# Optimization experiments

Hardware: AMD Instinct MI355X
Metric: run time of the kernel (lower is better)

## Reference

```python
import jax, jax.numpy as jnp
import numpy as np

N_NODES = 50000
N_EDGES = 800000
IN_CH = 128
HID = 128
OUT_CH = 16
N_LAYERS = 3
N_GRAPHS = 128
BN_EPS = 1e-5


def setup_inputs() -> dict:
    key = jax.random.key(0)
    ks = jax.random.split(key, 12)
    x = jax.random.normal(ks[0], (N_NODES, IN_CH), dtype=jnp.float32)
    edge_index = jax.random.randint(ks[1], (2, N_EDGES), 0, N_NODES, dtype=jnp.int64)
    batch = jnp.sort(jax.random.randint(ks[2], (N_NODES,), 0, N_GRAPHS, dtype=jnp.int64))
    s = 1.0 / np.sqrt(HID)
    W1 = jax.random.normal(ks[3], (N_LAYERS, IN_CH, HID), dtype=jnp.float32) * s
    b1 = jax.random.normal(ks[4], (N_LAYERS, HID), dtype=jnp.float32) * s
    W2 = jax.random.normal(ks[5], (N_LAYERS, HID, HID), dtype=jnp.float32) * s
    b2 = jax.random.normal(ks[6], (N_LAYERS, HID), dtype=jnp.float32) * s
    gamma = jnp.ones((N_LAYERS, HID), dtype=jnp.float32)
    beta = jnp.zeros((N_LAYERS, HID), dtype=jnp.float32)
    mean = jax.random.normal(ks[7], (N_LAYERS, HID), dtype=jnp.float32) * 0.1
    var = jax.random.uniform(ks[8], (N_LAYERS, HID), dtype=jnp.float32, minval=0.5, maxval=1.5)
    Wc = jax.random.normal(ks[9], (HID, OUT_CH), dtype=jnp.float32) * s
    bc = jax.random.normal(ks[10], (OUT_CH,), dtype=jnp.float32) * s
    return {"x": x, "edge_index": edge_index, "batch": batch, "W1": W1, "b1": b1,
            "W2": W2, "b2": b2, "gamma": gamma, "beta": beta, "mean": mean,
            "var": var, "Wc": Wc, "bc": bc}


def reference(x, edge_index, batch, W1, b1, W2, b2, gamma, beta, mean, var, Wc, bc):
    # GIN (eval mode: BN uses running stats, dropout is identity).
    src, dst = edge_index[0], edge_index[1]
    n = x.shape[0]
    h = x
    for i in range(N_LAYERS):
        # GINConv with eps=0: MLP(x + sum_{j->i} x_j)
        agg = jax.ops.segment_sum(h[src], dst, num_segments=n)  # [N, d]
        z = h + agg
        z = jnp.maximum(z @ W1[i] + b1[i], 0.0) @ W2[i] + b2[i]  # 2-layer MLP
        # BatchNorm1d (eval) + ReLU
        inv = gamma[i] * jax.lax.rsqrt(var[i] + BN_EPS)
        h = jnp.maximum((z - mean[i]) * inv + beta[i], 0.0)
    pooled = jax.ops.segment_sum(h, batch, num_segments=N_GRAPHS)  # [G, hid]
    return pooled @ Wc + bc
```

## Files before the change

kernel.cpp:

```cpp
#include <hip/hip_runtime.h>

#define N_NODES 50000
#define N_EDGES 800000
#define CH 128
#define N_GRAPHS 128
#define N_LAYERS 3
#define OUT_CH 16
#define BN_EPS 1e-5f
#define NSPLIT 32
#define NB 196
#define BCAP 4608
#define EPB 4096
#define NTILES (N_NODES / 16)
#define SSTRIDE 20
#define CB 6250
#define SB 196
#define PB 388

typedef unsigned short ushort_t;
typedef __attribute__((ext_vector_type(8))) short bf16x8;
typedef __attribute__((ext_vector_type(4))) float f32x4;

__device__ inline ushort_t f2b(float f) {
    unsigned u = __float_as_uint(f);
    unsigned r = (u + 0x7fffu + ((u >> 16) & 1u)) >> 16;
    return (ushort_t)r;
}
__device__ inline float blo(unsigned u) { return __uint_as_float(u << 16); }
__device__ inline float bhi(unsigned u) { return __uint_as_float(u & 0xffff0000u); }

__global__ __launch_bounds__(256) void setup_kernel(
    const float4* __restrict__ x, ushort4* __restrict__ xb, int* __restrict__ gcur,
    const int* __restrict__ batch, int* __restrict__ starts, float* __restrict__ outinit,
    const float* __restrict__ bc,
    const float* __restrict__ W1, const float* __restrict__ W2, ushort_t* __restrict__ Wt,
    const float* __restrict__ b1, const float* __restrict__ b2,
    const float* __restrict__ gamma, const float* __restrict__ beta,
    const float* __restrict__ mean, const float* __restrict__ var,
    float* __restrict__ scale, float* __restrict__ shift) {
    int bid = blockIdx.x, t = threadIdx.x;
    if (bid < CB) {
        int i = bid * 256 + t;
        if (i < NB) gcur[i] = 0;
        float4 v = x[i];
        ushort4 o;
        o.x = f2b(v.x); o.y = f2b(v.y); o.z = f2b(v.z); o.w = f2b(v.w);
        xb[i] = o;
    } else if (bid < CB + SB) {
        int i = (bid - CB) * 256 + t;
        if (i < N_GRAPHS * OUT_CH) outinit[i] = bc[i & (OUT_CH - 1)];
        if (i >= N_NODES) return;
        int b = batch[i];
        if (i == 0) {
            for (int g = 0; g <= b; ++g) starts[g] = 0;
        } else {
            int pb = batch[i - 1];
            for (int g = pb + 1; g <= b; ++g) starts[g] = i;
        }
        if (i == N_NODES - 1) {
            for (int g = b + 1; g <= N_GRAPHS; ++g) starts[g] = N_NODES;
        }
    } else {
        int i = (bid - CB - SB) * 256 + t;
        if (i < 6 * CH * CH) {
            int mat = i >> 14, r = i & 16383;
            int j = r & 7, bb = r >> 3;
            int lane = bb & 63, cs = bb >> 6;
            int ct = cs >> 2, ks = cs & 3;
            int n = ct * 16 + (lane & 15);
            int k = ks * 32 + (lane >> 4) * 8 + j;
            const float* Wsrc = (mat < 3) ? (W1 + (size_t)mat * CH * CH)
                                          : (W2 + (size_t)(mat - 3) * CH * CH);
            Wt[i] = f2b(Wsrc[k * CH + n]);
        } else {
            int e = i - 6 * CH * CH;
            if (e >= 6 * CH) return;
            int mat = e / CH, c = e % CH;
            if (mat < 3) {
                scale[e] = 1.f;
                shift[e] = b1[mat * CH + c];
            } else {
                int l = mat - 3;
                float inv = gamma[l * CH + c] * rsqrtf(var[l * CH + c] + BN_EPS);
                scale[e] = inv;
                shift[e] = (b2[l * CH + c] - mean[l * CH + c]) * inv + beta[l * CH + c];
            }
        }
    }
}

__global__ __launch_bounds__(256) void bin_kernel(const int* __restrict__ src,
                                                  const int* __restrict__ dst,
                                                  int* __restrict__ gcur,
                                                  unsigned* __restrict__ gbuck) {
    __shared__ int lcnt[256];
    __shared__ int lpref[256];
    __shared__ int lpos[NB];
    __shared__ int lbase[NB];
    __shared__ unsigned stage[EPB];
    __shared__ unsigned char sbk[EPB];
    int t = threadIdx.x;
    int e0 = blockIdx.x * EPB;
    int nloc = N_EDGES - e0; if (nloc > EPB) nloc = EPB;

    lcnt[t] = 0;
    __syncthreads();

    int2 ed[16];
    #pragma unroll
    for (int j = 0; j < 16; ++j) {
        int i = j * 256 + t;
        if (i < nloc) {
            ed[j].x = src[e0 + i];
            ed[j].y = dst[e0 + i];
            atomicAdd(&lcnt[ed[j].y >> 8], 1);
        } else ed[j].y = -1;
    }
    __syncthreads();
    int v = lcnt[t];
    lpref[t] = v;
    __syncthreads();
    for (int off = 1; off < 256; off <<= 1) {
        int y = (t >= off) ? lpref[t - off] : 0;
        __syncthreads();
        lpref[t] += y;
        __syncthreads();
    }
    int excl = lpref[t] - v;
    __syncthreads();
    lpref[t] = excl;
    if (t < NB) {
        lpos[t] = excl;
        lbase[t] = atomicAdd(&gcur[t], v);
    }
    __syncthreads();
    #pragma unroll
    for (int j = 0; j < 16; ++j) {
        if (ed[j].y >= 0) {
            int b = ed[j].y >> 8;
            int slot = atomicAdd(&lpos[b], 1);
            stage[slot] = (unsigned)ed[j].x | ((unsigned)(ed[j].y & 255) << 16);
            sbk[slot] = (unsigned char)b;
        }
    }
    __syncthreads();
    for (int i = t; i < nloc; i += 256) {
        int b = sbk[i];
        gbuck[(size_t)b * BCAP + lbase[b] + (i - lpref[b])] = stage[i];
    }
}

__global__ __launch_bounds__(256) void place_kernel(const int* __restrict__ gcur,
                                                    const unsigned* __restrict__ gbuck,
                                                    int* __restrict__ rowptr,
                                                    ushort_t* __restrict__ esrc) {
    __shared__ ushort_t ssrc[BCAP];
    __shared__ unsigned char sd[BCAP];
    __shared__ int outS[BCAP];
    __shared__ int cnt[256], pref[256], cur[256];
    __shared__ int sscan[256];
    int b = blockIdx.x, t = threadIdx.x;
    int gv = (t < NB) ? gcur[t] : 0;
    sscan[t] = gv;
    cnt[t] = 0;
    __syncthreads();
    for (int off = 1; off < 256; off <<= 1) {
        int y = (t >= off) ? sscan[t - off] : 0;
        __syncthreads();
        sscan[t] += y;
        __syncthreads();
    }
    int nb = gcur[b];
    int base = sscan[b] - nb;
    for (int i = t; i < nb; i += 256) {
        unsigned p = gbuck[(size_t)b * BCAP + i];
        ssrc[i] = (ushort_t)(p & 0xffffu);
        int dl = (p >> 16) & 0xff;
        sd[i] = (unsigned char)dl;
        atomicAdd(&cnt[dl], 1);
    }
    __syncthreads();
    int v = cnt[t];
    pref[t] = v;
    __syncthreads();
    for (int off = 1; off < 256; off <<= 1) {
        int y = (t >= off) ? pref[t - off] : 0;
        __syncthreads();
        pref[t] += y;
        __syncthreads();
    }
    int excl = pref[t] - v;
    __syncthreads();
    pref[t] = excl;
    cur[t] = 0;
    int idx = (b << 8) + t;
    if (idx < N_NODES) rowptr[idx] = base + excl;
    if (b == NB - 1 && t == 0) rowptr[N_NODES] = N_EDGES;
    __syncthreads();
    for (int i = t; i < nb; i += 256) {
        int dl = sd[i];
        int p = pref[dl] + atomicAdd(&cur[dl], 1);
        outS[p] = ssrc[i];
    }
    __syncthreads();
    for (int i = t; i < nb; i += 256)
        esrc[base + i] = (ushort_t)outS[i];
}

__global__ __launch_bounds__(512, 8) void layer_kernel(
    const unsigned* __restrict__ h2, const int* __restrict__ rowptr,
    const ushort_t* __restrict__ esrc,
    const ushort_t* __restrict__ Wf1, const ushort_t* __restrict__ Wf2,
    const float* __restrict__ shift1, const float* __restrict__ scale2,
    const float* __restrict__ shift2, ushort_t* __restrict__ hout) {
    __shared__ unsigned zt[16][68];
    __shared__ ushort_t sS[CH * SSTRIDE];

    int t = threadIdx.x;
    int wave = t >> 6, lane = t & 63;
    int quad = lane >> 4, l16 = lane & 15;
    int row0 = blockIdx.x * 16;

    for (int nn = 0; nn < 2; ++nn) {
        int node = row0 + wave * 2 + nn;
        unsigned self = h2[(size_t)node * 64 + lane];
        float ax = blo(self), ay = bhi(self);
        int e = rowptr[node], end = rowptr[node + 1];
        for (; e + 16 <= end; e += 16) {
            unsigned u[16];
            #pragma unroll
            for (int j = 0; j < 16; ++j) {
                int s = esrc[e + j];
                u[j] = h2[(size_t)s * 64 + lane];
            }
            #pragma unroll
            for (int j = 0; j < 16; ++j) { ax += blo(u[j]); ay += bhi(u[j]); }
        }
        for (; e + 8 <= end; e += 8) {
            unsigned u[8];
            #pragma unroll
            for (int j = 0; j < 8; ++j) {
                int s = esrc[e + j];
                u[j] = h2[(size_t)s * 64 + lane];
            }
            #pragma unroll
            for (int j = 0; j < 8; ++j) { ax += blo(u[j]); ay += bhi(u[j]); }
        }
        for (; e + 4 <= end; e += 4) {
            unsigned u[4];
            #pragma unroll
            for (int j = 0; j < 4; ++j) {
                int s = esrc[e + j];
                u[j] = h2[(size_t)s * 64 + lane];
            }
            #pragma unroll
            for (int j = 0; j < 4; ++j) { ax += blo(u[j]); ay += bhi(u[j]); }
        }
        for (; e < end; ++e) {
            unsigned u = h2[(size_t)esrc[e] * 64 + lane];
            ax += blo(u); ay += bhi(u);
        }
        zt[wave * 2 + nn][lane] = ((unsigned)f2b(ay) << 16) | (unsigned)f2b(ax);
    }
    __syncthreads();

    {
        bf16x8 af[4];
        #pragma unroll
        for (int ks = 0; ks < 4; ++ks)
            af[ks] = *(const bf16x8*)((const ushort_t*)&zt[l16][0] + ks * 32 + quad * 8);
        bf16x8 w1[4];
        #pragma unroll
        for (int ks = 0; ks < 4; ++ks)
            w1[ks] = *(const bf16x8*)(Wf1 + ((size_t)(wave * 4 + ks) * 64 + lane) * 8);
        f32x4 acc = (f32x4){0.f, 0.f, 0.f, 0.f};
        #pragma unroll
        for (int ks = 0; ks < 4; ++ks)
            acc = __builtin_amdgcn_mfma_f32_16x16x32_bf16(af[ks], w1[ks], acc, 0, 0, 0);
        int k = wave * 16 + l16;
        float sh = shift1[k];
        uint2 p;
        p.x = ((unsigned)f2b(fmaxf(acc[1] + sh, 0.f)) << 16)
            |  (unsigned)f2b(fmaxf(acc[0] + sh, 0.f));
        p.y = ((unsigned)f2b(fmaxf(acc[3] + sh, 0.f)) << 16)
            |  (unsigned)f2b(fmaxf(acc[2] + sh, 0.f));
        *(uint2*)&sS[k * SSTRIDE + quad * 4] = p;
    }
    __syncthreads();

    {
        bf16x8 af2[4];
        #pragma unroll
        for (int ks = 0; ks < 4; ++ks)
            #pragma unroll
            for (int j = 0; j < 8; ++j)
                af2[ks][j] = (short)sS[(ks * 32 + quad * 8 + j) * SSTRIDE + l16];
        bf16x8 w2[4];
        #pragma unroll
        for (int ks = 0; ks < 4; ++ks)
            w2[ks] = *(const bf16x8*)(Wf2 + ((size_t)(wave * 4 + ks) * 64 + lane) * 8);
        f32x4 acc = (f32x4){0.f, 0.f, 0.f, 0.f};
        #pragma unroll
        for (int ks = 0; ks < 4; ++ks)
            acc = __builtin_amdgcn_mfma_f32_16x16x32_bf16(af2[ks], w2[ks], acc, 0, 0, 0);
        int col = wave * 16 + l16;
        float sc = scale2[col], sh = shift2[col];
        #pragma unroll
        for (int r = 0; r < 4; ++r) {
            int row = row0 + quad * 4 + r;
            hout[(size_t)row * CH + col] = f2b(fmaxf(acc[r] * sc + sh, 0.f));
        }
    }
}

__global__ __launch_bounds__(64) void pool_kernel(const unsigned* __restrict__ h2,
                                                  const int* __restrict__ starts,
                                                  const float* __restrict__ Wc,
                                                  float* __restrict__ out) {
    int g = blockIdx.x / NSPLIT, s = blockIdx.x % NSPLIT;
    int c = threadIdx.x;
    int beg = starts[g], end = starts[g + 1];
    float s0 = 0.f, s1 = 0.f;
    for (int n = beg + s; n < end; n += NSPLIT) {
        unsigned u = h2[(size_t)n * 64 + c];
        s0 += blo(u); s1 += bhi(u);
    }
    float p[OUT_CH];
    #pragma unroll
    for (int o = 0; o < OUT_CH; ++o)
        p[o] = s0 * Wc[(2 * c) * OUT_CH + o] + s1 * Wc[(2 * c + 1) * OUT_CH + o];
    #pragma unroll
    for (int o = 0; o < OUT_CH; ++o) {
        p[o] += __shfl_xor(p[o], 1);
        p[o] += __shfl_xor(p[o], 2);
        p[o] += __shfl_xor(p[o], 4);
        p[o] += __shfl_xor(p[o], 8);
        p[o] += __shfl_xor(p[o], 16);
        p[o] += __shfl_xor(p[o], 32);
    }
    if (c == 0) {
        #pragma unroll
        for (int o = 0; o < OUT_CH; ++o)
            atomicAdd(&out[g * OUT_CH + o], p[o]);
    }
}

extern "C" void kernel_launch(void* const* d_in, const int* in_sizes, int n_in,
                              void* d_out, int out_size, void* d_ws, size_t ws_size,
                              hipStream_t stream) {
    const float* x     = (const float*)d_in[0];
    const int*   eidx  = (const int*)d_in[1];
    const int*   batch = (const int*)d_in[2];
    const float* W1    = (const float*)d_in[3];
    const float* b1    = (const float*)d_in[4];
    const float* W2    = (const float*)d_in[5];
    const float* b2    = (const float*)d_in[6];
    const float* gamma = (const float*)d_in[7];
    const float* beta  = (const float*)d_in[8];
    const float* mean  = (const float*)d_in[9];
    const float* var   = (const float*)d_in[10];
    const float* Wc    = (const float*)d_in[11];
    const float* bc    = (const float*)d_in[12];
    float* out = (float*)d_out;

    const int* src = eidx;
    const int* dst = eidx + N_EDGES;

    char* w = (char*)d_ws;
    size_t off = 0;
    auto alloc = [&](size_t bytes) { void* p = w + off; off += (bytes + 255) & ~(size_t)255; return p; };
    int*      gcur   = (int*)alloc(NB * 4);
    unsigned* gbuck  = (unsigned*)alloc((size_t)NB * BCAP * 4);
    int*      rowptr = (int*)alloc((N_NODES + 1) * 4);
    ushort_t* esrc   = (ushort_t*)alloc(N_EDGES * 2);
    int*      starts = (int*)alloc((N_GRAPHS + 1) * 4);
    ushort_t* Bh     = (ushort_t*)alloc((size_t)N_NODES * CH * 2);
    ushort_t* Bz     = (ushort_t*)alloc((size_t)N_NODES * CH * 2);
    ushort_t* Wt     = (ushort_t*)alloc((size_t)6 * CH * CH * 2);
    float*    scale  = (float*)alloc(6 * CH * 4);
    float*    shift  = (float*)alloc(6 * CH * 4);
    (void)ws_size; (void)n_in; (void)in_sizes; (void)out_size;

    setup_kernel<<<CB + SB + PB, 256, 0, stream>>>(
        (const float4*)x, (ushort4*)Bh, gcur,
        batch, starts, out, bc,
        W1, W2, Wt, b1, b2, gamma, beta, mean, var, scale, shift);
    bin_kernel<<<(N_EDGES + EPB - 1) / EPB, 256, 0, stream>>>(src, dst, gcur, gbuck);
    place_kernel<<<NB, 256, 0, stream>>>(gcur, gbuck, rowptr, esrc);

    ushort_t* bufA = Bh;
    ushort_t* bufB = Bz;
    for (int i = 0; i < N_LAYERS; ++i) {
        layer_kernel<<<NTILES, 512, 0, stream>>>((const unsigned*)bufA, rowptr, esrc,
                                                 Wt + (size_t)i * CH * CH,
                                                 Wt + (size_t)(3 + i) * CH * CH,
                                                 shift + i * CH,
                                                 scale + (3 + i) * CH,
                                                 shift + (3 + i) * CH,
                                                 bufB);
        ushort_t* tmp = bufA; bufA = bufB; bufB = tmp;
    }

    pool_kernel<<<N_GRAPHS * NSPLIT, 64, 0, stream>>>((const unsigned*)bufA, starts, Wc, out);
}
```

Before: 269.4 us.

## Fuse graph pooling into last GIN layer and interleave two-node gather

The last layer kernel now accumulates its post-BN activations straight into a per-graph pooled buffer with atomics, skipping the bf16 write of the final hidden state. A small classifier kernel then applies Wc and bc, which replaces the starts-based pool kernel and the starts setup. The neighbour gather now processes both of a wave's nodes in one interleaved loop with predicated 16-wide batches, so more loads are in flight. The pooling path adds float atomics and depends on batch being sorted for its fast path, and the predicated loads may raise register pressure.

```diff
diff --git a/kernel.cpp b/kernel.cpp
--- a/kernel.cpp
+++ b/kernel.cpp
@@ -7,7 +7,6 @@
 #define N_LAYERS 3
 #define OUT_CH 16
 #define BN_EPS 1e-5f
-#define NSPLIT 32
 #define NB 196
 #define BCAP 4608
 #define EPB 4096
@@ -31,8 +30,7 @@
 
 __global__ __launch_bounds__(256) void setup_kernel(
     const float4* __restrict__ x, ushort4* __restrict__ xb, int* __restrict__ gcur,
-    const int* __restrict__ batch, int* __restrict__ starts, float* __restrict__ outinit,
-    const float* __restrict__ bc,
+    float* __restrict__ pooled,
     const float* __restrict__ W1, const float* __restrict__ W2, ushort_t* __restrict__ Wt,
     const float* __restrict__ b1, const float* __restrict__ b2,
     const float* __restrict__ gamma, const float* __restrict__ beta,
@@ -42,26 +40,13 @@
     if (bid < CB) {
         int i = bid * 256 + t;
         if (i < NB) gcur[i] = 0;
+        if (i < N_GRAPHS * CH) pooled[i] = 0.f;
         float4 v = x[i];
         ushort4 o;
         o.x = f2b(v.x); o.y = f2b(v.y); o.z = f2b(v.z); o.w = f2b(v.w);
         xb[i] = o;
-    } else if (bid < CB + SB) {
+    } else {
         int i = (bid - CB) * 256 + t;
-        if (i < N_GRAPHS * OUT_CH) outinit[i] = bc[i & (OUT_CH - 1)];
-        if (i >= N_NODES) return;
-        int b = batch[i];
-        if (i == 0) {
-            for (int g = 0; g <= b; ++g) starts[g] = 0;
-        } else {
-            int pb = batch[i - 1];
-            for (int g = pb + 1; g <= b; ++g) starts[g] = i;
-        }
-        if (i == N_NODES - 1) {
-            for (int g = b + 1; g <= N_GRAPHS; ++g) starts[g] = N_NODES;
-        }
-    } else {
-        int i = (bid - CB - SB) * 256 + t;
         if (i < 6 * CH * CH) {
             int mat = i >> 14, r = i & 16383;
             int j = r & 7, bb = r >> 3;
@@ -212,7 +197,8 @@
     const ushort_t* __restrict__ esrc,
     const ushort_t* __restrict__ Wf1, const ushort_t* __restrict__ Wf2,
     const float* __restrict__ shift1, const float* __restrict__ scale2,
-    const float* __restrict__ shift2, ushort_t* __restrict__ hout) {
+    const float* __restrict__ shift2, ushort_t* __restrict__ hout,
+    const int* __restrict__ batch, float* __restrict__ pooled, int do_pool) {
     __shared__ unsigned zt[16][68];
     __shared__ ushort_t sS[CH * SSTRIDE];
 
@@ -221,46 +207,35 @@
     int quad = lane >> 4, l16 = lane & 15;
     int row0 = blockIdx.x * 16;
 
-    for (int nn = 0; nn < 2; ++nn) {
-        int node = row0 + wave * 2 + nn;
-        unsigned self = h2[(size_t)node * 64 + lane];
-        float ax = blo(self), ay = bhi(self);
-        int e = rowptr[node], end = rowptr[node + 1];
-        for (; e + 16 <= end; e += 16) {
-            unsigned u[16];
-            #pragma unroll
-            for (int j = 0; j < 16; ++j) {
-                int s = esrc[e + j];
-                u[j] = h2[(size_t)s * 64 + lane];
-            }
-            #pragma unroll
-            for (int j = 0; j < 16; ++j) { ax += blo(u[j]); ay += bhi(u[j]); }
+    {
+        int nodeA = row0 + wave * 2;
+        int nodeB = nodeA + 1;
+        unsigned selfA = h2[(size_t)nodeA * 64 + lane];
+        unsigned selfB = h2[(size_t)nodeB * 64 + lane];
+        float axA = blo(selfA), ayA = bhi(selfA);
+        float axB = blo(selfB), ayB = bhi(selfB);
+        int eA = rowptr[nodeA], endA = rowptr[nodeA + 1];
+        int eB = rowptr[nodeB], endB = rowptr[nodeB + 1];
+        while (eA < endA || eB < endB) {
+            int nA = endA - eA; if (nA > 16) nA = 16;
+            int nB = endB - eB; if (nB > 16) nB = 16;
+            unsigned uA[16], uB[16];
+            #pragma unroll
+            for (int j = 0; j < 16; ++j)
+                if (j < nA) uA[j] = h2[(size_t)esrc[eA + j] * 64 + lane];
+            #pragma unroll
+            for (int j = 0; j < 16; ++j)
+                if (j < nB) uB[j] = h2[(size_t)esrc[eB + j] * 64 + lane];
+            #pragma unroll
+            for (int j = 0; j < 16; ++j)
+                if (j < nA) { axA += blo(uA[j]); ayA += bhi(uA[j]); }
+            #pragma unroll
+            for (int j = 0; j < 16; ++j)
+                if (j < nB) { axB += blo(uB[j]); ayB += bhi(uB[j]); }
+            eA += nA; eB += nB;
         }
-        for (; e + 8 <= end; e += 8) {
-            unsigned u[8];
-            #pragma unroll
-            for (int j = 0; j < 8; ++j) {
-                int s = esrc[e + j];
-                u[j] = h2[(size_t)s * 64 + lane];
-            }
-            #pragma unroll
-            for (int j = 0; j < 8; ++j) { ax += blo(u[j]); ay += bhi(u[j]); }
-        }
-        for (; e + 4 <= end; e += 4) {
-            unsigned u[4];
-            #pragma unroll
-            for (int j = 0; j < 4; ++j) {
-                int s = esrc[e + j];
-                u[j] = h2[(size_t)s * 64 + lane];
-            }
-            #pragma unroll
-            for (int j = 0; j < 4; ++j) { ax += blo(u[j]); ay += bhi(u[j]); }
-        }
-        for (; e < end; ++e) {
-            unsigned u = h2[(size_t)esrc[e] * 64 + lane];
-            ax += blo(u); ay += bhi(u);
-        }
-        zt[wave * 2 + nn][lane] = ((unsigned)f2b(ay) << 16) | (unsigned)f2b(ax);
+        zt[wave * 2][lane]     = ((unsigned)f2b(ayA) << 16) | (unsigned)f2b(axA);
+        zt[wave * 2 + 1][lane] = ((unsigned)f2b(ayB) << 16) | (unsigned)f2b(axB);
     }
     __syncthreads();
 
@@ -305,44 +280,44 @@
             acc = __builtin_amdgcn_mfma_f32_16x16x32_bf16(af2[ks], w2[ks], acc, 0, 0, 0);
         int col = wave * 16 + l16;
         float sc = scale2[col], sh = shift2[col];
-        #pragma unroll
-        for (int r = 0; r < 4; ++r) {
-            int row = row0 + quad * 4 + r;
-            hout[(size_t)row * CH + col] = f2b(fmaxf(acc[r] * sc + sh, 0.f));
+        float hv[4];
+        #pragma unroll
+        for (int r = 0; r < 4; ++r)
+            hv[r] = fmaxf(acc[r] * sc + sh, 0.f);
+        if (!do_pool) {
+            #pragma unroll
+            for (int r = 0; r < 4; ++r) {
+                int row = row0 + quad * 4 + r;
+                hout[(size_t)row * CH + col] = f2b(hv[r]);
+            }
+        } else {
+            int g0 = batch[row0], g15 = batch[row0 + 15];
+            if (g0 == g15) {
+                float s = hv[0] + hv[1] + hv[2] + hv[3];
+                s += __shfl_xor(s, 16);
+                s += __shfl_xor(s, 32);
+                if (quad == 0) atomicAdd(&pooled[g0 * CH + col], s);
+            } else {
+                #pragma unroll
+                for (int r = 0; r < 4; ++r) {
+                    int row = row0 + quad * 4 + r;
+                    atomicAdd(&pooled[batch[row] * CH + col], hv[r]);
+                }
+            }
         }
     }
 }
 
-__global__ __launch_bounds__(64) void pool_kernel(const unsigned* __restrict__ h2,
-                                                  const int* __restrict__ starts,
+__global__ __launch_bounds__(256) void cls_kernel(const float* __restrict__ pooled,
                                                   const float* __restrict__ Wc,
+                                                  const float* __restrict__ bc,
                                                   float* __restrict__ out) {
-    int g = blockIdx.x / NSPLIT, s = blockIdx.x % NSPLIT;
-    int c = threadIdx.x;
-    int beg = starts[g], end = starts[g + 1];
-    float s0 = 0.f, s1 = 0.f;
-    for (int n = beg + s; n < end; n += NSPLIT) {
-        unsigned u = h2[(size_t)n * 64 + c];
-        s0 += blo(u); s1 += bhi(u);
-    }
-    float p[OUT_CH];
-    #pragma unroll
-    for (int o = 0; o < OUT_CH; ++o)
-        p[o] = s0 * Wc[(2 * c) * OUT_CH + o] + s1 * Wc[(2 * c + 1) * OUT_CH + o];
-    #pragma unroll
-    for (int o = 0; o < OUT_CH; ++o) {
-        p[o] += __shfl_xor(p[o], 1);
-        p[o] += __shfl_xor(p[o], 2);
-        p[o] += __shfl_xor(p[o], 4);
-        p[o] += __shfl_xor(p[o], 8);
-        p[o] += __shfl_xor(p[o], 16);
-        p[o] += __shfl_xor(p[o], 32);
-    }
-    if (c == 0) {
-        #pragma unroll
-        for (int o = 0; o < OUT_CH; ++o)
-            atomicAdd(&out[g * OUT_CH + o], p[o]);
-    }
+    int i = blockIdx.x * blockDim.x + threadIdx.x;
+    if (i >= N_GRAPHS * OUT_CH) return;
+    int g = i / OUT_CH, o = i % OUT_CH;
+    float s = bc[o];
+    for (int k = 0; k < CH; ++k) s += pooled[g * CH + k] * Wc[k * OUT_CH + o];
+    out[i] = s;
 }
 
 extern "C" void kernel_launch(void* const* d_in, const int* in_sizes, int n_in,
@@ -373,17 +348,16 @@
     unsigned* gbuck  = (unsigned*)alloc((size_t)NB * BCAP * 4);
     int*      rowptr = (int*)alloc((N_NODES + 1) * 4);
     ushort_t* esrc   = (ushort_t*)alloc(N_EDGES * 2);
-    int*      starts = (int*)alloc((N_GRAPHS + 1) * 4);
     ushort_t* Bh     = (ushort_t*)alloc((size_t)N_NODES * CH * 2);
     ushort_t* Bz     = (ushort_t*)alloc((size_t)N_NODES * CH * 2);
     ushort_t* Wt     = (ushort_t*)alloc((size_t)6 * CH * CH * 2);
     float*    scale  = (float*)alloc(6 * CH * 4);
     float*    shift  = (float*)alloc(6 * CH * 4);
+    float*    pooled = (float*)alloc(N_GRAPHS * CH * 4);
     (void)ws_size; (void)n_in; (void)in_sizes; (void)out_size;
 
-    setup_kernel<<<CB + SB + PB, 256, 0, stream>>>(
-        (const float4*)x, (ushort4*)Bh, gcur,
-        batch, starts, out, bc,
+    setup_kernel<<<CB + PB, 256, 0, stream>>>(
+        (const float4*)x, (ushort4*)Bh, gcur, pooled,
         W1, W2, Wt, b1, b2, gamma, beta, mean, var, scale, shift);
     bin_kernel<<<(N_EDGES + EPB - 1) / EPB, 256, 0, stream>>>(src, dst, gcur, gbuck);
     place_kernel<<<NB, 256, 0, stream>>>(gcur, gbuck, rowptr, esrc);
@@ -391,15 +365,16 @@
     ushort_t* bufA = Bh;
     ushort_t* bufB = Bz;
     for (int i = 0; i < N_LAYERS; ++i) {
+        int last = (i == N_LAYERS - 1);
         layer_kernel<<<NTILES, 512, 0, stream>>>((const unsigned*)bufA, rowptr, esrc,
                                                  Wt + (size_t)i * CH * CH,
                                                  Wt + (size_t)(3 + i) * CH * CH,
                                                  shift + i * CH,
                                                  scale + (3 + i) * CH,
                                                  shift + (3 + i) * CH,
-                                                 bufB);
+                                                 bufB, batch, pooled, last);
         ushort_t* tmp = bufA; bufA = bufB; bufB = tmp;
     }
 
-    pool_kernel<<<N_GRAPHS * NSPLIT, 64, 0, stream>>>((const unsigned*)bufA, starts, Wc, out);
-}
+    cls_kernel<<<(N_GRAPHS * OUT_CH + 255) / 256, 256, 0, stream>>>(pooled, Wc, bc, out);
+}
```

Result: slower. 337.2 us (+25.1%).
